# Optimization experiments

Hardware: AMD Instinct MI355X
Metric: run time of the kernel (lower is better)

## Reference

```python
import jax, jax.numpy as jnp
import numpy as np

LN_EPS = 1e-5

def _layernorm(x, g, b):
    m = jnp.mean(x, axis=-1, keepdims=True)
    v = jnp.mean((x - m) ** 2, axis=-1, keepdims=True)
    return (x - m) / jnp.sqrt(v + LN_EPS) * g + b

def _mlp(x, w1, g1, b1, w2, g2, b2):
    # Linear(no bias) -> LayerNorm -> Linear(no bias) -> LayerNorm -> ReLU
    x = _layernorm(x @ w1, g1, b1)
    x = _layernorm(x @ w2, g2, b2)
    return jax.nn.relu(x)

def setup_inputs() -> dict:
    key = jax.random.key(0)
    ks = jax.random.split(key, 16)
    Lc, Lf, N, Dc, Df, K = 1024, 4096, 32, 256, 128, 8
    inv = lambda d: 1.0 / np.sqrt(d)
    inp = {
        "features_coarse": jax.random.normal(ks[0], (Lc, N, Dc), dtype=jnp.float32),
        "features_fine": jax.random.normal(ks[1], (Lf, N, Df), dtype=jnp.float32),
        # mlp_coarse: d_in=Dc, d_ff=Df, d_out=Df
        "w1c": jax.random.uniform(ks[2], (Dc, Df), jnp.float32, -inv(Dc), inv(Dc)),
        "g1c": jnp.ones((Df,), jnp.float32),
        "b1c": jnp.zeros((Df,), jnp.float32),
        "w2c": jax.random.uniform(ks[3], (Df, Df), jnp.float32, -inv(Df), inv(Df)),
        "g2c": jnp.ones((Df,), jnp.float32),
        "b2c": jnp.zeros((Df,), jnp.float32),
        # mlp_fine: d_in=Df, d_ff=Df, d_out=Df
        "w1f": jax.random.uniform(ks[4], (Df, Df), jnp.float32, -inv(Df), inv(Df)),
        "g1f": jnp.ones((Df,), jnp.float32),
        "b1f": jnp.zeros((Df,), jnp.float32),
        "w2f": jax.random.uniform(ks[5], (Df, Df), jnp.float32, -inv(Df), inv(Df)),
        "g2f": jnp.ones((Df,), jnp.float32),
        "b2f": jnp.zeros((Df,), jnp.float32),
        "neighbor_row": jax.random.randint(ks[6], (K * Lc * N,), 0, Lf, dtype=jnp.int64 if jax.config.jax_enable_x64 else jnp.int32),
        "neighbor_col": jax.random.randint(ks[7], (K * Lc * N,), 0, N, dtype=jnp.int64 if jax.config.jax_enable_x64 else jnp.int32),
        "keep_idx": jax.random.randint(ks[8], (Lc,), 0, Lf, dtype=jnp.int64 if jax.config.jax_enable_x64 else jnp.int32),
    }
    return inp

def reference(features_coarse, features_fine, w1c, g1c, b1c, w2c, g2c, b2c,
              w1f, g1f, b1f, w2f, g2f, b2f, neighbor_row, neighbor_col, keep_idx):
    Lc, N, Dc = features_coarse.shape
    Lf, _, Df = features_fine.shape
    D = Df
    fc = _mlp(features_coarse, w1c, g1c, b1c, w2c, g2c, b2c)  # (Lc, N, D)
    ff = _mlp(features_fine, w1f, g1f, b1f, w2f, g2f, b2f)    # (Lf, N, D)
    gathered = ff[neighbor_row, neighbor_col]                  # (K*Lc*N, D)
    updated = fc[None] + gathered.reshape(-1, Lc, N, D)        # (K, Lc, N, D)
    ff = ff.at[neighbor_row, neighbor_col].set(updated.reshape(-1, D))
    return ff
```

## Files before the change

### kernel.cpp

```cpp
#include <hip/hip_runtime.h>
#include <hip/hip_bf16.h>

typedef __attribute__((ext_vector_type(8))) short s8v;
typedef __attribute__((ext_vector_type(4))) float f4v;

__device__ __forceinline__ short f2bf(float f) {
    __hip_bfloat16 h = __float2bfloat16(f);
    union { __hip_bfloat16 h; short s; } u{h};
    return u.s;
}
__device__ __forceinline__ float bf2f(unsigned short v) {
    union { unsigned u; float f; } x; x.u = ((unsigned)v) << 16; return x.f;
}

__global__ void prep_kernel(const int* __restrict__ nr, const int* __restrict__ nc,
                            int* __restrict__ win,
                            const float* __restrict__ w1c, const float* __restrict__ w2c,
                            const float* __restrict__ w1f, const float* __restrict__ w2f,
                            short* __restrict__ p1c, short* __restrict__ p2c,
                            short* __restrict__ p1f, short* __restrict__ p2f)
{
    int b = blockIdx.x, t = threadIdx.x;
    if (b < 1024) {
        int i = b * 256 + t;
        atomicMax(&win[nr[i] * 32 + nc[i]], i);
        return;
    }
    int id = (b - 1024) * 256 + t;
    int f  = id >> 6, l = id & 63;
    const float* W; short* P; int fl;
    if      (f < 64)  { W = w1c; P = p1c; fl = f; }
    else if (f < 96)  { W = w2c; P = p2c; fl = f - 64; }
    else if (f < 128) { W = w1f; P = p1f; fl = f - 96; }
    else              { W = w2f; P = p2f; fl = f - 128; }
    int g = l >> 4, c = l & 15;
    int ks = fl >> 3, n = fl & 7;
    s8v o;
    #pragma unroll
    for (int e = 0; e < 8; ++e)
        o[e] = f2bf(W[(ks*32 + g*8 + e) * 128 + n*16 + c]);
    *(s8v*)(P + ((fl*64 + l) << 3)) = o;
}

template<int K1, bool FINE>
__global__ __launch_bounds__(256, 4)
void mlp_mfma(const float* __restrict__ X,
              const short* __restrict__ Wp1,
              const float* __restrict__ g1v, const float* __restrict__ b1v,
              const short* __restrict__ Wp2,
              const float* __restrict__ g2v, const float* __restrict__ b2v,
              float* __restrict__ outF,
              unsigned short* __restrict__ outB,
              const int* __restrict__ winner,
              const unsigned short* __restrict__ fcB)
{
    __shared__ short H1L[4][16][136];

    const int t = threadIdx.x;
    const int wave = t >> 6, lane = t & 63;
    const int g = lane >> 4, c = lane & 15;
    const int wrow = blockIdx.x * 64 + wave * 16;

    f4v acc[8];
    #pragma unroll
    for (int n = 0; n < 8; ++n) acc[n] = (f4v){0.f, 0.f, 0.f, 0.f};

    #pragma unroll
    for (int ks = 0; ks < K1/32; ++ks) {
        s8v af;
        {
            const float* p = X + (size_t)(wrow + c) * K1 + ks*32 + g*8;
            float4 a0 = *(const float4*)p;
            float4 a1 = *(const float4*)(p + 4);
            af[0] = f2bf(a0.x); af[1] = f2bf(a0.y); af[2] = f2bf(a0.z); af[3] = f2bf(a0.w);
            af[4] = f2bf(a1.x); af[5] = f2bf(a1.y); af[6] = f2bf(a1.z); af[7] = f2bf(a1.w);
        }
        #pragma unroll
        for (int n = 0; n < 8; ++n) {
            s8v bf = *(const s8v*)(Wp1 + (((ks*8 + n)*64 + lane) << 3));
            acc[n] = __builtin_amdgcn_mfma_f32_16x16x32_bf16(af, bf, acc[n], 0, 0, 0);
        }
    }

    {
        float G[8], B[8];
        #pragma unroll
        for (int n = 0; n < 8; ++n) { G[n] = g1v[n*16 + c]; B[n] = b1v[n*16 + c]; }
        #pragma unroll
        for (int j = 0; j < 4; ++j) {
            float sm = 0.f, sq = 0.f;
            #pragma unroll
            for (int n = 0; n < 8; ++n) { float v = acc[n][j]; sm += v; sq += v*v; }
            #pragma unroll
            for (int m = 1; m < 16; m <<= 1) {
                sm += __shfl_xor(sm, m, 64);
                sq += __shfl_xor(sq, m, 64);
            }
            float mean = sm * (1.f/128.f);
            float rstd = rsqrtf(sq * (1.f/128.f) - mean*mean + 1e-5f);
            int row = g*4 + j;
            #pragma unroll
            for (int n = 0; n < 8; ++n) {
                float y = (acc[n][j] - mean) * rstd * G[n] + B[n];
                H1L[wave][row][(n*16 + c) ^ (g << 3)] = f2bf(y);
            }
        }
    }

    f4v acc2[8];
    #pragma unroll
    for (int n = 0; n < 8; ++n) acc2[n] = (f4v){0.f, 0.f, 0.f, 0.f};

    const int rg = (c >> 2) & 3;
    #pragma unroll
    for (int ks = 0; ks < 4; ++ks) {
        s8v af = *(const s8v*)&H1L[wave][c][(ks*32 + g*8) ^ (rg << 3)];
        #pragma unroll
        for (int n = 0; n < 8; ++n) {
            s8v bf = *(const s8v*)(Wp2 + (((ks*8 + n)*64 + lane) << 3));
            acc2[n] = __builtin_amdgcn_mfma_f32_16x16x32_bf16(af, bf, acc2[n], 0, 0, 0);
        }
    }

    {
        float G[8], B[8];
        #pragma unroll
        for (int n = 0; n < 8; ++n) { G[n] = g2v[n*16 + c]; B[n] = b2v[n*16 + c]; }
        #pragma unroll
        for (int j = 0; j < 4; ++j) {
            float sm = 0.f, sq = 0.f;
            #pragma unroll
            for (int n = 0; n < 8; ++n) { float v = acc2[n][j]; sm += v; sq += v*v; }
            #pragma unroll
            for (int m = 1; m < 16; m <<= 1) {
                sm += __shfl_xor(sm, m, 64);
                sq += __shfl_xor(sq, m, 64);
            }
            float mean = sm * (1.f/128.f);
            float rstd = rsqrtf(sq * (1.f/128.f) - mean*mean + 1e-5f);
            int R = wrow + g*4 + j;
            float y[8];
            #pragma unroll
            for (int n = 0; n < 8; ++n)
                y[n] = fmaxf((acc2[n][j] - mean) * rstd * G[n] + B[n], 0.f);
            if constexpr (FINE) {
                int w = winner[R];
                if (w >= 0) {
                    int src = w & 32767;
                    const unsigned short* fp = fcB + (size_t)src * 128 + c;
                    #pragma unroll
                    for (int n = 0; n < 8; ++n) y[n] += bf2f(fp[n*16]);
                }
                float* op = outF + (size_t)R * 128 + c;
                #pragma unroll
                for (int n = 0; n < 8; ++n) op[n*16] = y[n];
            } else {
                unsigned short* op = outB + (size_t)R * 128 + c;
                #pragma unroll
                for (int n = 0; n < 8; ++n) op[n*16] = (unsigned short)f2bf(y[n]);
            }
        }
    }
}

extern "C" void kernel_launch(void* const* d_in, const int* in_sizes, int n_in,
                              void* d_out, int out_size, void* d_ws, size_t ws_size,
                              hipStream_t stream)
{
    const float* fcoarse = (const float*)d_in[0];
    const float* ffine   = (const float*)d_in[1];
    const float* w1c = (const float*)d_in[2];
    const float* g1c = (const float*)d_in[3];
    const float* b1c = (const float*)d_in[4];
    const float* w2c = (const float*)d_in[5];
    const float* g2c = (const float*)d_in[6];
    const float* b2c = (const float*)d_in[7];
    const float* w1f = (const float*)d_in[8];
    const float* g1f = (const float*)d_in[9];
    const float* b1f = (const float*)d_in[10];
    const float* w2f = (const float*)d_in[11];
    const float* g2f = (const float*)d_in[12];
    const float* b2f = (const float*)d_in[13];
    const int* nrow  = (const int*)d_in[14];
    const int* ncol  = (const int*)d_in[15];

    float* out = (float*)d_out;

    const int Mc = 32768, Mf = 131072;

    unsigned short* fcB = (unsigned short*)d_ws;
    char* base = (char*)d_ws;
    int*   winner = (int*)(base + 8u*1024*1024);
    short* p1c = (short*)(base + 8u*1024*1024 + 512u*1024);
    short* p2c = p1c + 256*128;
    short* p1f = p2c + 128*128;
    short* p2f = p1f + 128*128;

    hipMemsetAsync(winner, 0xFF, (size_t)Mf * sizeof(int), stream);
    prep_kernel<<<1064, 256, 0, stream>>>(nrow, ncol, winner,
                                          w1c, w2c, w1f, w2f,
                                          p1c, p2c, p1f, p2f);

    mlp_mfma<256, false><<<Mc/64, 256, 0, stream>>>(fcoarse, p1c, g1c, b1c,
                                                    p2c, g2c, b2c,
                                                    nullptr, fcB, nullptr, nullptr);
    mlp_mfma<128, true><<<Mf/64, 256, 0, stream>>>(ffine, p1f, g1f, b1f,
                                                   p2f, g2f, b2f,
                                                   out, nullptr, winner, fcB);
}
```

Measured before the change: 86.40 us.

## Stage MLP epilogue through LDS for vectorized row stores and prefetch inputs

```diff
diff --git a/kernel.cpp b/kernel.cpp
--- a/kernel.cpp
+++ b/kernel.cpp
@@ -2,6 +2,7 @@
 #include <hip/hip_bf16.h>
 
 typedef __attribute__((ext_vector_type(8))) short s8v;
+typedef __attribute__((ext_vector_type(8))) unsigned short u8v;
 typedef __attribute__((ext_vector_type(4))) float f4v;
 
 __device__ __forceinline__ short f2bf(float f) {
@@ -61,20 +62,33 @@
     const int g = lane >> 4, c = lane & 15;
     const int wrow = blockIdx.x * 64 + wave * 16;
 
+    int wv = 0;
+    if constexpr (FINE) wv = winner[wrow + c];
+
+    float G1[8], B1[8], G2[8], B2[8];
+    #pragma unroll
+    for (int n = 0; n < 8; ++n) {
+        G1[n] = g1v[n*16 + c]; B1[n] = b1v[n*16 + c];
+        G2[n] = g2v[n*16 + c]; B2[n] = b2v[n*16 + c];
+    }
+
     f4v acc[8];
     #pragma unroll
     for (int n = 0; n < 8; ++n) acc[n] = (f4v){0.f, 0.f, 0.f, 0.f};
 
+    const float* pa = X + (size_t)(wrow + c) * K1 + g*8;
+    float4 a0 = *(const float4*)pa;
+    float4 a1 = *(const float4*)(pa + 4);
     #pragma unroll
     for (int ks = 0; ks < K1/32; ++ks) {
+        float4 c0 = a0, c1 = a1;
+        if (ks + 1 < K1/32) {
+            a0 = *(const float4*)(pa + (ks+1)*32);
+            a1 = *(const float4*)(pa + (ks+1)*32 + 4);
+        }
         s8v af;
-        {
-            const float* p = X + (size_t)(wrow + c) * K1 + ks*32 + g*8;
-            float4 a0 = *(const float4*)p;
-            float4 a1 = *(const float4*)(p + 4);
-            af[0] = f2bf(a0.x); af[1] = f2bf(a0.y); af[2] = f2bf(a0.z); af[3] = f2bf(a0.w);
-            af[4] = f2bf(a1.x); af[5] = f2bf(a1.y); af[6] = f2bf(a1.z); af[7] = f2bf(a1.w);
-        }
+        af[0] = f2bf(c0.x); af[1] = f2bf(c0.y); af[2] = f2bf(c0.z); af[3] = f2bf(c0.w);
+        af[4] = f2bf(c1.x); af[5] = f2bf(c1.y); af[6] = f2bf(c1.z); af[7] = f2bf(c1.w);
         #pragma unroll
         for (int n = 0; n < 8; ++n) {
             s8v bf = *(const s8v*)(Wp1 + (((ks*8 + n)*64 + lane) << 3));
@@ -82,28 +96,23 @@
         }
     }
 
-    {
-        float G[8], B[8];
-        #pragma unroll
-        for (int n = 0; n < 8; ++n) { G[n] = g1v[n*16 + c]; B[n] = b1v[n*16 + c]; }
-        #pragma unroll
-        for (int j = 0; j < 4; ++j) {
-            float sm = 0.f, sq = 0.f;
-            #pragma unroll
-            for (int n = 0; n < 8; ++n) { float v = acc[n][j]; sm += v; sq += v*v; }
-            #pragma unroll
-            for (int m = 1; m < 16; m <<= 1) {
-                sm += __shfl_xor(sm, m, 64);
-                sq += __shfl_xor(sq, m, 64);
-            }
-            float mean = sm * (1.f/128.f);
-            float rstd = rsqrtf(sq * (1.f/128.f) - mean*mean + 1e-5f);
-            int row = g*4 + j;
-            #pragma unroll
-            for (int n = 0; n < 8; ++n) {
-                float y = (acc[n][j] - mean) * rstd * G[n] + B[n];
-                H1L[wave][row][(n*16 + c) ^ (g << 3)] = f2bf(y);
-            }
+    #pragma unroll
+    for (int j = 0; j < 4; ++j) {
+        float sm = 0.f, sq = 0.f;
+        #pragma unroll
+        for (int n = 0; n < 8; ++n) { float v = acc[n][j]; sm += v; sq += v*v; }
+        #pragma unroll
+        for (int m = 1; m < 16; m <<= 1) {
+            sm += __shfl_xor(sm, m, 64);
+            sq += __shfl_xor(sq, m, 64);
+        }
+        float mean = sm * (1.f/128.f);
+        float rstd = rsqrtf(sq * (1.f/128.f) - mean*mean + 1e-5f);
+        int row = g*4 + j;
+        #pragma unroll
+        for (int n = 0; n < 8; ++n) {
+            float y = (acc[n][j] - mean) * rstd * G1[n] + B1[n];
+            H1L[wave][row][(n*16 + c) ^ (g << 3)] = f2bf(y);
         }
     }
 
@@ -122,43 +131,49 @@
         }
     }
 
-    {
-        float G[8], B[8];
-        #pragma unroll
-        for (int n = 0; n < 8; ++n) { G[n] = g2v[n*16 + c]; B[n] = b2v[n*16 + c]; }
-        #pragma unroll
-        for (int j = 0; j < 4; ++j) {
-            float sm = 0.f, sq = 0.f;
+    #pragma unroll
+    for (int j = 0; j < 4; ++j) {
+        float sm = 0.f, sq = 0.f;
+        #pragma unroll
+        for (int n = 0; n < 8; ++n) { float v = acc2[n][j]; sm += v; sq += v*v; }
+        #pragma unroll
+        for (int m = 1; m < 16; m <<= 1) {
+            sm += __shfl_xor(sm, m, 64);
+            sq += __shfl_xor(sq, m, 64);
+        }
+        float mean = sm * (1.f/128.f);
+        float rstd = rsqrtf(sq * (1.f/128.f) - mean*mean + 1e-5f);
+        int row = g*4 + j;
+        #pragma unroll
+        for (int n = 0; n < 8; ++n) {
+            float y = fmaxf((acc2[n][j] - mean) * rstd * G2[n] + B2[n], 0.f);
+            H1L[wave][row][(n*16 + c) ^ (g << 3)] = f2bf(y);
+        }
+    }
+
+    const int c8 = lane & 15;
+    #pragma unroll
+    for (int it = 0; it < 4; ++it) {
+        int row = it*4 + (lane >> 4);
+        int R   = wrow + row;
+        s8v v = *(const s8v*)&H1L[wave][row][(c8 ^ it) * 8];
+        if constexpr (FINE) {
+            float y8[8];
             #pragma unroll
-            for (int n = 0; n < 8; ++n) { float v = acc2[n][j]; sm += v; sq += v*v; }
-            #pragma unroll
-            for (int m = 1; m < 16; m <<= 1) {
-                sm += __shfl_xor(sm, m, 64);
-                sq += __shfl_xor(sq, m, 64);
+            for (int e = 0; e < 8; ++e) y8[e] = bf2f((unsigned short)v[e]);
+            int w = __shfl(wv, row, 64);
+            if (w >= 0) {
+                const u8v u = *(const u8v*)(fcB + (size_t)(w & 32767) * 128 + c8*8);
+                #pragma unroll
+                for (int e = 0; e < 8; ++e) y8[e] += bf2f(u[e]);
             }
-            float mean = sm * (1.f/128.f);
-            float rstd = rsqrtf(sq * (1.f/128.f) - mean*mean + 1e-5f);
-            int R = wrow + g*4 + j;
-            float y[8];
-            #pragma unroll
-            for (int n = 0; n < 8; ++n)
-                y[n] = fmaxf((acc2[n][j] - mean) * rstd * G[n] + B[n], 0.f);
-            if constexpr (FINE) {
-                int w = winner[R];
-                if (w >= 0) {
-                    int src = w & 32767;
-                    const unsigned short* fp = fcB + (size_t)src * 128 + c;
-                    #pragma unroll
-                    for (int n = 0; n < 8; ++n) y[n] += bf2f(fp[n*16]);
-                }
-                float* op = outF + (size_t)R * 128 + c;
-                #pragma unroll
-                for (int n = 0; n < 8; ++n) op[n*16] = y[n];
-            } else {
-                unsigned short* op = outB + (size_t)R * 128 + c;
-                #pragma unroll
-                for (int n = 0; n < 8; ++n) op[n*16] = (unsigned short)f2bf(y[n]);
-            }
+            float4 o0 = {y8[0], y8[1], y8[2], y8[3]};
+            float4 o1 = {y8[4], y8[5], y8[6], y8[7]};
+            float* op = outF + (size_t)R * 128 + c8*8;
+            *(float4*)op       = o0;
+            *(float4*)(op + 4) = o1;
+        } else {
+            *(s8v*)(outB + (size_t)R * 128 + c8*8) = v;
         }
     }
 }
```

Measured after the change: 92.61 us. 7.2% more time.

## Fold winner atomics into coarse MLP launch and prefetch operands

Applied to the files above, without the earlier changes.

```diff
diff --git a/kernel.cpp b/kernel.cpp
--- a/kernel.cpp
+++ b/kernel.cpp
@@ -13,20 +13,12 @@
     union { unsigned u; float f; } x; x.u = ((unsigned)v) << 16; return x.f;
 }
 
-__global__ void prep_kernel(const int* __restrict__ nr, const int* __restrict__ nc,
-                            int* __restrict__ win,
-                            const float* __restrict__ w1c, const float* __restrict__ w2c,
+__global__ void pack_kernel(const float* __restrict__ w1c, const float* __restrict__ w2c,
                             const float* __restrict__ w1f, const float* __restrict__ w2f,
                             short* __restrict__ p1c, short* __restrict__ p2c,
                             short* __restrict__ p1f, short* __restrict__ p2f)
 {
-    int b = blockIdx.x, t = threadIdx.x;
-    if (b < 1024) {
-        int i = b * 256 + t;
-        atomicMax(&win[nr[i] * 32 + nc[i]], i);
-        return;
-    }
-    int id = (b - 1024) * 256 + t;
+    int id = blockIdx.x * 256 + threadIdx.x;
     int f  = id >> 6, l = id & 63;
     const float* W; short* P; int fl;
     if      (f < 64)  { W = w1c; P = p1c; fl = f; }
@@ -52,113 +44,130 @@
               float* __restrict__ outF,
               unsigned short* __restrict__ outB,
               const int* __restrict__ winner,
-              const unsigned short* __restrict__ fcB)
+              const unsigned short* __restrict__ fcB,
+              const int* __restrict__ nr, const int* __restrict__ nc,
+              int* __restrict__ win, int nWinBlocks)
 {
-    __shared__ short H1L[4][16][136];
+    __shared__ short H[4][16][128];
+
+    if (blockIdx.x < (unsigned)nWinBlocks) {
+        int i = blockIdx.x * 256 + threadIdx.x;
+        atomicMax(&win[nr[i] * 32 + nc[i]], i);
+        return;
+    }
+    const int bid = blockIdx.x - nWinBlocks;
 
     const int t = threadIdx.x;
     const int wave = t >> 6, lane = t & 63;
     const int g = lane >> 4, c = lane & 15;
-    const int wrow = blockIdx.x * 64 + wave * 16;
+    const int wrow = bid * 64 + wave * 16;
+
+    int wv = 0;
+    if constexpr (FINE) wv = winner[wrow + c];
+
+    float G1[8], B1[8];
+    #pragma unroll
+    for (int n = 0; n < 8; ++n) { G1[n] = g1v[n*16 + c]; B1[n] = b1v[n*16 + c]; }
 
     f4v acc[8];
     #pragma unroll
     for (int n = 0; n < 8; ++n) acc[n] = (f4v){0.f, 0.f, 0.f, 0.f};
 
+    const float* pa = X + (size_t)(wrow + c) * K1 + g*8;
+    const short* wp1 = Wp1 + (lane << 3);
+    float4 a0 = *(const float4*)pa;
+    float4 a1 = *(const float4*)(pa + 4);
     #pragma unroll
     for (int ks = 0; ks < K1/32; ++ks) {
+        s8v bfr[8];
+        #pragma unroll
+        for (int n = 0; n < 8; ++n)
+            bfr[n] = *(const s8v*)(wp1 + ((ks*8 + n) << 9));
         s8v af;
-        {
-            const float* p = X + (size_t)(wrow + c) * K1 + ks*32 + g*8;
-            float4 a0 = *(const float4*)p;
-            float4 a1 = *(const float4*)(p + 4);
-            af[0] = f2bf(a0.x); af[1] = f2bf(a0.y); af[2] = f2bf(a0.z); af[3] = f2bf(a0.w);
-            af[4] = f2bf(a1.x); af[5] = f2bf(a1.y); af[6] = f2bf(a1.z); af[7] = f2bf(a1.w);
-        }
+        af[0] = f2bf(a0.x); af[1] = f2bf(a0.y); af[2] = f2bf(a0.z); af[3] = f2bf(a0.w);
+        af[4] = f2bf(a1.x); af[5] = f2bf(a1.y); af[6] = f2bf(a1.z); af[7] = f2bf(a1.w);
+        if (ks + 1 < K1/32) {
+            a0 = *(const float4*)(pa + (ks+1)*32);
+            a1 = *(const float4*)(pa + (ks+1)*32 + 4);
+        }
+        #pragma unroll
+        for (int n = 0; n < 8; ++n)
+            acc[n] = __builtin_amdgcn_mfma_f32_16x16x32_bf16(af, bfr[n], acc[n], 0, 0, 0);
+    }
+
+    #pragma unroll
+    for (int j = 0; j < 4; ++j) {
+        float sm = 0.f, sq = 0.f;
+        #pragma unroll
+        for (int n = 0; n < 8; ++n) { float v = acc[n][j]; sm += v; sq += v*v; }
+        #pragma unroll
+        for (int m = 1; m < 16; m <<= 1) {
+            sm += __shfl_xor(sm, m, 64);
+            sq += __shfl_xor(sq, m, 64);
+        }
+        float mean = sm * (1.f/128.f);
+        float rstd = rsqrtf(sq * (1.f/128.f) - mean*mean + 1e-5f);
+        int row = g*4 + j;
         #pragma unroll
         for (int n = 0; n < 8; ++n) {
-            s8v bf = *(const s8v*)(Wp1 + (((ks*8 + n)*64 + lane) << 3));
-            acc[n] = __builtin_amdgcn_mfma_f32_16x16x32_bf16(af, bf, acc[n], 0, 0, 0);
-        }
-    }
-
-    {
-        float G[8], B[8];
-        #pragma unroll
-        for (int n = 0; n < 8; ++n) { G[n] = g1v[n*16 + c]; B[n] = b1v[n*16 + c]; }
-        #pragma unroll
-        for (int j = 0; j < 4; ++j) {
-            float sm = 0.f, sq = 0.f;
+            float y = (acc[n][j] - mean) * rstd * G1[n] + B1[n];
+            int col = n*16 + c;
+            int phys = (((col >> 3) ^ row) << 3) | (col & 7);
+            H[wave][row][phys] = f2bf(y);
+        }
+    }
+
+    f4v acc2[8];
+    #pragma unroll
+    for (int n = 0; n < 8; ++n) acc2[n] = (f4v){0.f, 0.f, 0.f, 0.f};
+
+    const short* wp2 = Wp2 + (lane << 3);
+    #pragma unroll
+    for (int ks = 0; ks < 4; ++ks) {
+        s8v bfr[8];
+        #pragma unroll
+        for (int n = 0; n < 8; ++n)
+            bfr[n] = *(const s8v*)(wp2 + ((ks*8 + n) << 9));
+        s8v af = *(const s8v*)&H[wave][c][((ks*4 + g) ^ c) << 3];
+        #pragma unroll
+        for (int n = 0; n < 8; ++n)
+            acc2[n] = __builtin_amdgcn_mfma_f32_16x16x32_bf16(af, bfr[n], acc2[n], 0, 0, 0);
+    }
+
+    float G2[8], B2[8];
+    #pragma unroll
+    for (int n = 0; n < 8; ++n) { G2[n] = g2v[n*16 + c]; B2[n] = b2v[n*16 + c]; }
+    #pragma unroll
+    for (int j = 0; j < 4; ++j) {
+        float sm = 0.f, sq = 0.f;
+        #pragma unroll
+        for (int n = 0; n < 8; ++n) { float v = acc2[n][j]; sm += v; sq += v*v; }
+        #pragma unroll
+        for (int m = 1; m < 16; m <<= 1) {
+            sm += __shfl_xor(sm, m, 64);
+            sq += __shfl_xor(sq, m, 64);
+        }
+        float mean = sm * (1.f/128.f);
+        float rstd = rsqrtf(sq * (1.f/128.f) - mean*mean + 1e-5f);
+        int R = wrow + g*4 + j;
+        float y[8];
+        #pragma unroll
+        for (int n = 0; n < 8; ++n)
+            y[n] = fmaxf((acc2[n][j] - mean) * rstd * G2[n] + B2[n], 0.f);
+        if constexpr (FINE) {
+            int w = __shfl(wv, g*4 + j, 64);
+            if (w >= 0) {
+                const unsigned short* fp = fcB + (size_t)(w & 32767) * 128 + c;
+                #pragma unroll
+                for (int n = 0; n < 8; ++n) y[n] += bf2f(fp[n*16]);
+            }
+            float* op = outF + (size_t)R * 128 + c;
             #pragma unroll
-            for (int n = 0; n < 8; ++n) { float v = acc[n][j]; sm += v; sq += v*v; }
+            for (int n = 0; n < 8; ++n) op[n*16] = y[n];
+        } else {
+            unsigned short* op = outB + (size_t)R * 128 + c;
             #pragma unroll
-            for (int m = 1; m < 16; m <<= 1) {
-                sm += __shfl_xor(sm, m, 64);
-                sq += __shfl_xor(sq, m, 64);
-            }
-            float mean = sm * (1.f/128.f);
-            float rstd = rsqrtf(sq * (1.f/128.f) - mean*mean + 1e-5f);
-            int row = g*4 + j;
-            #pragma unroll
-            for (int n = 0; n < 8; ++n) {
-                float y = (acc[n][j] - mean) * rstd * G[n] + B[n];
-                H1L[wave][row][(n*16 + c) ^ (g << 3)] = f2bf(y);
-            }
-        }
-    }
-
-    f4v acc2[8];
-    #pragma unroll
-    for (int n = 0; n < 8; ++n) acc2[n] = (f4v){0.f, 0.f, 0.f, 0.f};
-
-    const int rg = (c >> 2) & 3;
-    #pragma unroll
-    for (int ks = 0; ks < 4; ++ks) {
-        s8v af = *(const s8v*)&H1L[wave][c][(ks*32 + g*8) ^ (rg << 3)];
-        #pragma unroll
-        for (int n = 0; n < 8; ++n) {
-            s8v bf = *(const s8v*)(Wp2 + (((ks*8 + n)*64 + lane) << 3));
-            acc2[n] = __builtin_amdgcn_mfma_f32_16x16x32_bf16(af, bf, acc2[n], 0, 0, 0);
-        }
-    }
-
-    {
-        float G[8], B[8];
-        #pragma unroll
-        for (int n = 0; n < 8; ++n) { G[n] = g2v[n*16 + c]; B[n] = b2v[n*16 + c]; }
-        #pragma unroll
-        for (int j = 0; j < 4; ++j) {
-            float sm = 0.f, sq = 0.f;
-            #pragma unroll
-            for (int n = 0; n < 8; ++n) { float v = acc2[n][j]; sm += v; sq += v*v; }
-            #pragma unroll
-            for (int m = 1; m < 16; m <<= 1) {
-                sm += __shfl_xor(sm, m, 64);
-                sq += __shfl_xor(sq, m, 64);
-            }
-            float mean = sm * (1.f/128.f);
-            float rstd = rsqrtf(sq * (1.f/128.f) - mean*mean + 1e-5f);
-            int R = wrow + g*4 + j;
-            float y[8];
-            #pragma unroll
-            for (int n = 0; n < 8; ++n)
-                y[n] = fmaxf((acc2[n][j] - mean) * rstd * G[n] + B[n], 0.f);
-            if constexpr (FINE) {
-                int w = winner[R];
-                if (w >= 0) {
-                    int src = w & 32767;
-                    const unsigned short* fp = fcB + (size_t)src * 128 + c;
-                    #pragma unroll
-                    for (int n = 0; n < 8; ++n) y[n] += bf2f(fp[n*16]);
-                }
-                float* op = outF + (size_t)R * 128 + c;
-                #pragma unroll
-                for (int n = 0; n < 8; ++n) op[n*16] = y[n];
-            } else {
-                unsigned short* op = outB + (size_t)R * 128 + c;
-                #pragma unroll
-                for (int n = 0; n < 8; ++n) op[n*16] = (unsigned short)f2bf(y[n]);
-            }
+            for (int n = 0; n < 8; ++n) op[n*16] = (unsigned short)f2bf(y[n]);
         }
     }
 }
@@ -197,14 +206,15 @@
     short* p2f = p1f + 128*128;
 
     hipMemsetAsync(winner, 0xFF, (size_t)Mf * sizeof(int), stream);
-    prep_kernel<<<1064, 256, 0, stream>>>(nrow, ncol, winner,
-                                          w1c, w2c, w1f, w2f,
-                                          p1c, p2c, p1f, p2f);
-
-    mlp_mfma<256, false><<<Mc/64, 256, 0, stream>>>(fcoarse, p1c, g1c, b1c,
-                                                    p2c, g2c, b2c,
-                                                    nullptr, fcB, nullptr, nullptr);
-    mlp_mfma<128, true><<<Mf/64, 256, 0, stream>>>(ffine, p1f, g1f, b1f,
-                                                   p2f, g2f, b2f,
-                                                   out, nullptr, winner, fcB);
-}
+    pack_kernel<<<40, 256, 0, stream>>>(w1c, w2c, w1f, w2f, p1c, p2c, p1f, p2f);
+
+    mlp_mfma<256, false><<<1024 + Mc/64, 256, 0, stream>>>(
+        fcoarse, p1c, g1c, b1c, p2c, g2c, b2c,
+        nullptr, fcB, nullptr, nullptr,
+        nrow, ncol, winner, 1024);
+
+    mlp_mfma<128, true><<<Mf/64, 256, 0, stream>>>(
+        ffine, p1f, g1f, b1f, p2f, g2f, b2f,
+        out, nullptr, winner, fcB,
+        nullptr, nullptr, nullptr, 0);
+}
```

Result: faster. 81.04 us (-6.2%).
